# Performance work log

Measured on AMD Instinct MI355X. Metric: run time of the kernel, lower is better.

Reference implementation:

```python
import jax, jax.numpy as jnp
import numpy as np

NUM_HEADS = 16
THETA = 10000.0


def _rope(x, pos):
    # x: (B, H, S, d_k), pos: (B, S) int
    d_k = x.shape[-1]
    freqs = 1.0 / (THETA ** (jnp.arange(0, d_k, 2, dtype=jnp.float32) / d_k))  # (d_k/2,)
    angles = pos[..., None].astype(jnp.float32) * freqs  # (B, S, d_k/2)
    cos = jnp.cos(angles)[:, None, :, :]  # (B, 1, S, d_k/2) broadcast over heads
    sin = jnp.sin(angles)[:, None, :, :]
    x1 = x[..., 0::2]
    x2 = x[..., 1::2]
    out1 = x1 * cos - x2 * sin
    out2 = x1 * sin + x2 * cos
    # interleave back: (..., d_k/2, 2) -> (..., d_k)
    return jnp.stack((out1, out2), axis=-1).reshape(x.shape)


def setup_inputs() -> dict:
    key = jax.random.key(0)
    ks = jax.random.split(key, 6)
    B, S, D = 4, 2048, 1024
    x = jax.random.normal(ks[0], (B, S, D), dtype=jnp.float32)
    token_positions = jnp.sort(jax.random.randint(ks[1], (B, S), 0, S), axis=-1).astype(jnp.int32)
    Wq = jax.random.normal(ks[2], (D, D), dtype=jnp.float32) * (D ** -0.5)
    Wk = jax.random.normal(ks[3], (D, D), dtype=jnp.float32) * (D ** -0.5)
    Wv = jax.random.normal(ks[4], (D, D), dtype=jnp.float32) * (D ** -0.5)
    Wo = jax.random.normal(ks[5], (D, D), dtype=jnp.float32) * (D ** -0.5)
    return {"x": x, "token_positions": token_positions, "Wq": Wq, "Wk": Wk, "Wv": Wv, "Wo": Wo}


def reference(x, token_positions, Wq, Wk, Wv, Wo):
    B, S, D = x.shape
    H = NUM_HEADS
    d_k = D // H
    # projections: y = x @ W.T  (Linear stores weight as (d_out, d_in))
    q = jnp.einsum('bsd,od->bso', x, Wq).reshape(B, S, H, d_k).transpose(0, 2, 1, 3)
    k = jnp.einsum('bsd,od->bso', x, Wk).reshape(B, S, H, d_k).transpose(0, 2, 1, 3)
    v = jnp.einsum('bsd,od->bso', x, Wv).reshape(B, S, H, d_k).transpose(0, 2, 1, 3)
    q = _rope(q, token_positions)
    k = _rope(k, token_positions)
    scores = jnp.einsum('bhqd,bhkd->bhqk', q, k) / jnp.sqrt(jnp.float32(d_k))
    causal = jnp.tril(jnp.ones((S, S), dtype=bool))
    scores = jnp.where(causal, scores, -jnp.inf)
    attn = jax.nn.softmax(scores, axis=-1)
    attn = jnp.nan_to_num(attn, nan=0.0)
    out = jnp.einsum('bhqk,bhkd->bhqd', attn, v)
    out = out.transpose(0, 2, 1, 3).reshape(B, S, D)
    return jnp.einsum('bso,do->bsd', out, Wo)
```

## Files before the change

kernel.cpp:

```cpp
#include <hip/hip_runtime.h>
#include <stdint.h>

#define SEQ 2048
#define NH  16
#define DK  64
#define DM  1024
#define C2SM 0.18033688011112042f

typedef __bf16 bf16x8 __attribute__((ext_vector_type(8)));
typedef float  f32x4  __attribute__((ext_vector_type(4)));
typedef float  f32x16 __attribute__((ext_vector_type(16)));
typedef int    iv2    __attribute__((ext_vector_type(2)));
typedef void __attribute__((address_space(3))) lds_void;
typedef const void __attribute__((address_space(1))) glb_void;

__device__ __forceinline__ unsigned short f2b(float f) {
  unsigned int u = __float_as_uint(f);
  u += 0x7fffu + ((u >> 16) & 1u);
  return (unsigned short)(u >> 16);
}
__device__ __forceinline__ float b2f(unsigned short h) {
  return __uint_as_float(((unsigned int)h) << 16);
}
__device__ __forceinline__ void gload_lds16(const void* g, void* lds) {
  __builtin_amdgcn_global_load_lds((glb_void*)(uintptr_t)g,
                                   (lds_void*)(unsigned int)(uintptr_t)lds,
                                   16, 0, 0);
}
__device__ __forceinline__ unsigned int cvtpk(float lo, float hi) {
  unsigned int r;
  asm("v_cvt_pk_bf16_f32 %0, %1, %2" : "=v"(r) : "v"(lo), "v"(hi));
  return r;
}
__device__ __forceinline__ iv2 pl32swap(int a, int b) {
  return __builtin_amdgcn_permlane32_swap(a, b, false, false);
}

__global__ __launch_bounds__(256) void k_prep(const float* __restrict__ x,
                                              const float* __restrict__ w0,
                                              const float* __restrict__ w1,
                                              const float* __restrict__ w2,
                                              const float* __restrict__ w3,
                                              unsigned short* __restrict__ xb,
                                              unsigned short* __restrict__ wb,
                                              float2* __restrict__ tab) {
  const int bid = blockIdx.x, tid = threadIdx.x;
  if (bid < 8192) {
    int i = bid * 256 + tid;
    float4 v = ((const float4*)x)[i];
    uint2 o;
    o.x = (unsigned int)f2b(v.x) | ((unsigned int)f2b(v.y) << 16);
    o.y = (unsigned int)f2b(v.z) | ((unsigned int)f2b(v.w) << 16);
    ((uint2*)xb)[i] = o;
  } else if (bid < 12288) {
    int i = (bid - 8192) * 256 + tid;
    const float* s = (i < 524288) ? ((i < 262144) ? w0 : w1)
                                  : ((i < 786432) ? w2 : w3);
    float4 v = ((const float4*)s)[i & 262143];
    uint2 o;
    o.x = (unsigned int)f2b(v.x) | ((unsigned int)f2b(v.y) << 16);
    o.y = (unsigned int)f2b(v.z) | ((unsigned int)f2b(v.w) << 16);
    ((uint2*)wb)[i] = o;
  } else {
    int i = (bid - 12288) * 256 + tid;
    int p = i >> 5, f = i & 31;
    float freq = powf(10000.0f, -(float)(2 * f) / (float)DK);
    float ang = (float)p * freq;
    tab[i] = make_float2(cosf(ang), sinf(ang));
  }
}

template <int MODE>
__global__ __launch_bounds__(256) void k_gemm(const unsigned short* __restrict__ A,
                                              const unsigned short* __restrict__ B,
                                              void* __restrict__ C, void* __restrict__ C2,
                                              const int* __restrict__ pos,
                                              const float2* __restrict__ tab,
                                              int M, int N, int K) {
  __shared__ __align__(16) unsigned short As[3][4096];
  __shared__ __align__(16) unsigned short Bs[3][4096];
  const int tid = threadIdx.x;
  const int wid = tid >> 6, lane = tid & 63;
  const int lr = lane & 15, lk = lane >> 4;
  const int wr = wid >> 1, wc = wid & 1;
  const int m0 = blockIdx.x * 128, n0 = blockIdx.y * 128;
  const int r0 = tid >> 2;
  const int csw = (((tid & 3) ^ ((r0 >> 1) & 3)) << 3);
  const int ss = ((lk ^ ((lr >> 1) & 3)) << 3);
  f32x4 acc[4][4] = {};

#define GSTAGE(bi, k0)                                                       \
  do {                                                                       \
    gload_lds16(A + (size_t)(m0 + r0) * K + (k0) + csw, &As[bi][wid * 512]); \
    gload_lds16(A + (size_t)(m0 + 64 + r0) * K + (k0) + csw,                 \
                &As[bi][2048 + wid * 512]);                                  \
    gload_lds16(B + (size_t)(n0 + r0) * K + (k0) + csw, &Bs[bi][wid * 512]); \
    gload_lds16(B + (size_t)(n0 + 64 + r0) * K + (k0) + csw,                 \
                &Bs[bi][2048 + wid * 512]);                                  \
  } while (0)

  const int nt = K >> 5;
  GSTAGE(0, 0);
  if (nt > 1) {
    GSTAGE(1, 32);
    asm volatile("s_waitcnt vmcnt(4)" ::: "memory");
  } else {
    asm volatile("s_waitcnt vmcnt(0)" ::: "memory");
  }
  __builtin_amdgcn_s_barrier();
  int c0 = 0, c1 = 1, c2 = 2;
  for (int t = 0; t < nt; ++t) {
    if (t + 2 < nt) GSTAGE(c2, (t + 2) * 32);
    bf16x8 af[4], bfv[4];
#pragma unroll
    for (int i = 0; i < 4; ++i)
      af[i] = *(const bf16x8*)&As[c0][(wr * 64 + i * 16 + lr) * 32 + ss];
#pragma unroll
    for (int j = 0; j < 4; ++j)
      bfv[j] = *(const bf16x8*)&Bs[c0][(wc * 64 + j * 16 + lr) * 32 + ss];
    __builtin_amdgcn_s_setprio(1);
#pragma unroll
    for (int i = 0; i < 4; ++i)
#pragma unroll
      for (int j = 0; j < 4; ++j)
        acc[i][j] = __builtin_amdgcn_mfma_f32_16x16x32_bf16(af[i], bfv[j], acc[i][j], 0, 0, 0);
    __builtin_amdgcn_s_setprio(0);
    if (t + 1 < nt) {
      if (t + 2 < nt)
        asm volatile("s_waitcnt vmcnt(4)" ::: "memory");
      else
        asm volatile("s_waitcnt vmcnt(0)" ::: "memory");
      __builtin_amdgcn_s_barrier();
    }
    int tmp = c0; c0 = c1; c1 = c2; c2 = tmp;
  }
#undef GSTAGE

  if (MODE == 1) {
#pragma unroll
    for (int i = 0; i < 4; ++i) {
      const int rbase = m0 + wr * 64 + i * 16 + lk * 4;
#pragma unroll
      for (int j = 0; j < 4; ++j) {
        const int col = n0 + wc * 64 + j * 16 + lr;
#pragma unroll
        for (int r = 0; r < 4; ++r)
          ((float*)C)[(size_t)(rbase + r) * N + col] = acc[i][j][r];
      }
    }
  } else {
    const int tt = n0 >> 10;
    if (tt == 2) {
#pragma unroll
      for (int i = 0; i < 4; ++i) {
        const int rbase = m0 + wr * 64 + i * 16 + lk * 4;
        const int bb = rbase >> 11;
        const int s0 = rbase & (SEQ - 1);
#pragma unroll
        for (int j = 0; j < 4; ++j) {
          const int col = n0 + wc * 64 + j * 16 + lr;
          const int h = (col >> 6) & 15, d = col & 63;
          uint2 pv;
          pv.x = cvtpk(acc[i][j][0], acc[i][j][1]);
          pv.y = cvtpk(acc[i][j][2], acc[i][j][3]);
          *(uint2*)&((unsigned short*)C2)[(((size_t)bb * NH + h) * DK + d) * SEQ + s0] = pv;
        }
      }
    } else {
#pragma unroll
      for (int i = 0; i < 4; ++i) {
        const int rbase = m0 + wr * 64 + i * 16 + lk * 4;
        const int bb = rbase >> 11;
        int prr[4];
#pragma unroll
        for (int r = 0; r < 4; ++r)
          prr[r] = pos[bb * SEQ + ((rbase + r) & (SEQ - 1))];
#pragma unroll
        for (int j = 0; j < 4; ++j) {
          const int col = n0 + wc * 64 + j * 16 + lr;
          const int h = (col >> 6) & 15, d = col & 63;
          const int f = d >> 1;
#pragma unroll
          for (int r = 0; r < 4; ++r) {
            float v = acc[i][j][r];
            float pv = __shfl_xor(v, 1);
            float2 cs = tab[(size_t)prr[r] * 32 + f];
            float o = (d & 1) ? __builtin_fmaf(pv, cs.y, v * cs.x)
                              : __builtin_fmaf(-pv, cs.y, v * cs.x);
            const int s = (rbase + r) & (SEQ - 1);
            ((unsigned short*)C)[(size_t)tt * 8388608 +
                                 ((((size_t)bb * NH + h) * SEQ) + s) * DK + d] = f2b(o);
          }
        }
      }
    }
  }
}

__global__ __launch_bounds__(128) void k_attn(const unsigned short* __restrict__ Q,
                                              const unsigned short* __restrict__ K,
                                              const unsigned short* __restrict__ VT,
                                              unsigned short* __restrict__ O) {
  __shared__ __align__(16) unsigned short Ks[2][64 * 64];
  __shared__ __align__(16) unsigned short Vs[2][64 * 64];
  const int tid = threadIdx.x, wid = tid >> 6, lane = tid & 63;
  const int l31 = lane & 31, hi = lane >> 5;
  const int n = blockIdx.x;
  const int bh = n & 63;
  const int qt = 31 - (n >> 6);
  const unsigned short* Qp = Q + (size_t)bh * SEQ * DK;
  const unsigned short* Kp = K + (size_t)bh * SEQ * DK;
  const unsigned short* Vp = VT + (size_t)bh * DK * SEQ;
  const int b = bh >> 4, h = bh & (NH - 1);

#define STAGE(bi, kb)                                                          \
  do {                                                                         \
    _Pragma("unroll") for (int i = 0; i < 4; ++i) {                            \
      const int c = i * 128 + tid;                                             \
      const int row = c >> 3, sl = ((c & 7) ^ (row & 7)) << 3;                 \
      gload_lds16(Kp + (size_t)((kb) + row) * DK + sl,                         \
                  &Ks[bi][(i * 128 + wid * 64) * 8]);                          \
      gload_lds16(Vp + (size_t)row * SEQ + (kb) + sl,                          \
                  &Vs[bi][(i * 128 + wid * 64) * 8]);                          \
    }                                                                          \
  } while (0)

  const int qw = qt * 64 + wid * 32;
  const int qrow = qw + l31;
  bf16x8 qf[4];
#pragma unroll
  for (int ks = 0; ks < 4; ++ks)
    qf[ks] = *(const bf16x8*)&Qp[(size_t)qrow * DK + ks * 16 + hi * 8];
  f32x16 oacc[2] = {};
  float m_ = -1e30f, l_ = 0.f;
  const int ntiles = qt + 1;
  STAGE(0, 0);
  for (int kt = 0; kt < ntiles; ++kt) {
    const int cur = kt & 1;
    const int kb = kt * 64;
    if (kt + 1 < ntiles) {
      STAGE(cur ^ 1, kb + 64);
      asm volatile("s_waitcnt vmcnt(8)" ::: "memory");
    } else {
      asm volatile("s_waitcnt vmcnt(0)" ::: "memory");
    }
    __builtin_amdgcn_s_barrier();
    {
      f32x16 sa[2];
      __builtin_amdgcn_s_setprio(1);
#pragma unroll
      for (int kg = 0; kg < 2; ++kg) {
        const int krow = kg * 32 + l31;
        f32x16 z = {};
#pragma unroll
        for (int ks = 0; ks < 4; ++ks) {
          bf16x8 kf = *(const bf16x8*)((const char*)&Ks[cur][0] + krow * 128 +
                                       (((2 * ks + hi) ^ (krow & 7)) << 4));
          z = __builtin_amdgcn_mfma_f32_32x32x16_bf16(kf, qf[ks], z, 0, 0, 0);
        }
        sa[kg] = z;
      }
      __builtin_amdgcn_s_setprio(0);
      if (kb + 64 > qw) {
        const int th0 = qrow - kb - 4 * hi;
#pragma unroll
        for (int kg = 0; kg < 2; ++kg) {
          const int th = th0 - kg * 32;
#pragma unroll
          for (int r = 0; r < 16; ++r) {
            const int cst = (r & 3) + 8 * (r >> 2);
            if (cst > th) sa[kg][r] = -1e30f;
          }
        }
      }
      float mx;
      {
        float a0 = fmaxf(fmaxf(sa[0][0], sa[0][1]), fmaxf(sa[0][2], sa[0][3]));
        float a1 = fmaxf(fmaxf(sa[0][4], sa[0][5]), fmaxf(sa[0][6], sa[0][7]));
        float a2 = fmaxf(fmaxf(sa[0][8], sa[0][9]), fmaxf(sa[0][10], sa[0][11]));
        float a3 = fmaxf(fmaxf(sa[0][12], sa[0][13]), fmaxf(sa[0][14], sa[0][15]));
        float a4 = fmaxf(fmaxf(sa[1][0], sa[1][1]), fmaxf(sa[1][2], sa[1][3]));
        float a5 = fmaxf(fmaxf(sa[1][4], sa[1][5]), fmaxf(sa[1][6], sa[1][7]));
        float a6 = fmaxf(fmaxf(sa[1][8], sa[1][9]), fmaxf(sa[1][10], sa[1][11]));
        float a7 = fmaxf(fmaxf(sa[1][12], sa[1][13]), fmaxf(sa[1][14], sa[1][15]));
        mx = fmaxf(fmaxf(fmaxf(a0, a1), fmaxf(a2, a3)),
                   fmaxf(fmaxf(a4, a5), fmaxf(a6, a7)));
        iv2 t = pl32swap(__float_as_int(mx), __float_as_int(mx));
        mx = fmaxf(__int_as_float(t.x), __int_as_float(t.y));
      }
      if (!__all(mx <= m_ + 16.f)) {
        const float mn = fmaxf(m_, mx);
        const float sc = __builtin_amdgcn_exp2f((m_ - mn) * C2SM);
        m_ = mn;
        l_ *= sc;
#pragma unroll
        for (int vg = 0; vg < 2; ++vg)
#pragma unroll
          for (int r = 0; r < 16; ++r) oacc[vg][r] *= sc;
      }
      const float mc = m_ * C2SM;
      float sum = 0.f;
#pragma unroll
      for (int kg = 0; kg < 2; ++kg)
#pragma unroll
        for (int r = 0; r < 16; ++r) {
          const float p = __builtin_amdgcn_exp2f(__builtin_fmaf(sa[kg][r], C2SM, -mc));
          sa[kg][r] = p;
          sum += p;
        }
      {
        iv2 t = pl32swap(__float_as_int(sum), __float_as_int(sum));
        l_ += __int_as_float(t.x) + __int_as_float(t.y);
      }
      __builtin_amdgcn_s_setprio(1);
#pragma unroll
      for (int kg = 0; kg < 2; ++kg)
#pragma unroll
        for (int ks2 = 0; ks2 < 2; ++ks2) {
          const int rb = ks2 * 8;
          unsigned wA = cvtpk(sa[kg][rb + 0], sa[kg][rb + 1]);
          unsigned wB = cvtpk(sa[kg][rb + 4], sa[kg][rb + 5]);
          unsigned wC = cvtpk(sa[kg][rb + 2], sa[kg][rb + 3]);
          unsigned wD = cvtpk(sa[kg][rb + 6], sa[kg][rb + 7]);
          iv2 r0 = pl32swap((int)wA, (int)wB);
          iv2 r1 = pl32swap((int)wC, (int)wD);
          union { uint4 u; bf16x8 v; } pu;
          pu.u = make_uint4((unsigned)r0.x, (unsigned)r1.x, (unsigned)r0.y, (unsigned)r1.y);
          const int ks = kg * 2 + ks2;
#pragma unroll
          for (int vg = 0; vg < 2; ++vg) {
            const int vrow = vg * 32 + l31;
            bf16x8 vf = *(const bf16x8*)((const char*)&Vs[cur][0] + vrow * 128 +
                                         (((2 * ks + hi) ^ (vrow & 7)) << 4));
            oacc[vg] = __builtin_amdgcn_mfma_f32_32x32x16_bf16(vf, pu.v, oacc[vg], 0, 0, 0);
          }
        }
      __builtin_amdgcn_s_setprio(0);
    }
    __builtin_amdgcn_s_barrier();
  }
  const float inv = 1.0f / l_;
  unsigned short* Orow = O + ((size_t)(b * SEQ + qrow)) * DM + h * DK;
#pragma unroll
  for (int vg = 0; vg < 2; ++vg)
#pragma unroll
    for (int j = 0; j < 4; ++j) {
      unsigned lo = cvtpk(oacc[vg][4 * j + 0] * inv, oacc[vg][4 * j + 1] * inv);
      unsigned hh = cvtpk(oacc[vg][4 * j + 2] * inv, oacc[vg][4 * j + 3] * inv);
      *(uint2*)&Orow[vg * 32 + 8 * j + 4 * hi] = make_uint2(lo, hh);
    }
#undef STAGE
}

extern "C" void kernel_launch(void* const* d_in, const int* in_sizes, int n_in,
                              void* d_out, int out_size, void* d_ws, size_t ws_size,
                              hipStream_t stream) {
  const float* x = (const float*)d_in[0];
  const int* tp = (const int*)d_in[1];
  const float* W[4] = {(const float*)d_in[2], (const float*)d_in[3],
                       (const float*)d_in[4], (const float*)d_in[5]};
  unsigned short* xb = (unsigned short*)d_ws;
  unsigned short* wb0 = xb + (size_t)8192 * 1024;
  unsigned short* wb3 = wb0 + (size_t)3 * 1024 * 1024;
  float2* tab = (float2*)(wb0 + (size_t)4 * 1024 * 1024);
  unsigned short* Qb = (unsigned short*)(tab + SEQ * 32);
  unsigned short* Kb = Qb + (size_t)8192 * 1024;
  unsigned short* VTb = Kb + (size_t)8192 * 1024;
  unsigned short* Ob = VTb + (size_t)8192 * 1024;

  k_prep<<<12544, 256, 0, stream>>>(x, W[0], W[1], W[2], W[3], xb, wb0, tab);
  k_gemm<3><<<dim3(64, 24), 256, 0, stream>>>(xb, wb0, Qb, VTb, tp, tab, 8192, 3072, 1024);
  k_attn<<<2048, 128, 0, stream>>>(Qb, Kb, VTb, Ob);
  k_gemm<1><<<dim3(64, 8), 256, 0, stream>>>(Ob, wb3, d_out, nullptr, nullptr, nullptr,
                                             8192, 1024, 1024);
}
```

Before: 176.3 us.

## Switch GEMM to BK=64 double-buffered tiles with 8-way XOR swizzle

Moves the projection GEMM from a triple-buffered K-tile of 32 to a double-buffered K-tile of 64, with a new 8-chunk XOR swizzle on the LDS layout. Each iteration now issues twice as many async global-to-LDS loads and runs two MFMA sub-steps per barrier, halving the number of barriers and waits. The cost is shallower prefetch: only one stage is in flight, and each iteration waits for all loads to finish (vmcnt(0)) before the next, which may expose memory latency.

```diff
diff --git a/kernel.cpp b/kernel.cpp
--- a/kernel.cpp
+++ b/kernel.cpp
@@ -77,62 +77,61 @@
                                               const int* __restrict__ pos,
                                               const float2* __restrict__ tab,
                                               int M, int N, int K) {
-  __shared__ __align__(16) unsigned short As[3][4096];
-  __shared__ __align__(16) unsigned short Bs[3][4096];
+  __shared__ __align__(16) unsigned short As[2][128 * 64];
+  __shared__ __align__(16) unsigned short Bs[2][128 * 64];
   const int tid = threadIdx.x;
   const int wid = tid >> 6, lane = tid & 63;
   const int lr = lane & 15, lk = lane >> 4;
   const int wr = wid >> 1, wc = wid & 1;
   const int m0 = blockIdx.x * 128, n0 = blockIdx.y * 128;
-  const int r0 = tid >> 2;
-  const int csw = (((tid & 3) ^ ((r0 >> 1) & 3)) << 3);
-  const int ss = ((lk ^ ((lr >> 1) & 3)) << 3);
   f32x4 acc[4][4] = {};
 
-#define GSTAGE(bi, k0)                                                       \
-  do {                                                                       \
-    gload_lds16(A + (size_t)(m0 + r0) * K + (k0) + csw, &As[bi][wid * 512]); \
-    gload_lds16(A + (size_t)(m0 + 64 + r0) * K + (k0) + csw,                 \
-                &As[bi][2048 + wid * 512]);                                  \
-    gload_lds16(B + (size_t)(n0 + r0) * K + (k0) + csw, &Bs[bi][wid * 512]); \
-    gload_lds16(B + (size_t)(n0 + 64 + r0) * K + (k0) + csw,                 \
-                &Bs[bi][2048 + wid * 512]);                                  \
+#define GSTAGE(bi, k0)                                                        \
+  do {                                                                        \
+    _Pragma("unroll") for (int rp = 0; rp < 4; ++rp) {                        \
+      const int c = rp * 256 + tid;                                           \
+      const int row = c >> 3;                                                 \
+      const int sl = ((c & 7) ^ (row & 7)) << 3;                              \
+      gload_lds16(A + (size_t)(m0 + row) * K + (k0) + sl,                     \
+                  &As[bi][(rp * 256 + wid * 64) * 8]);                        \
+      gload_lds16(B + (size_t)(n0 + row) * K + (k0) + sl,                     \
+                  &Bs[bi][(rp * 256 + wid * 64) * 8]);                        \
+    }                                                                         \
   } while (0)
 
-  const int nt = K >> 5;
+  const int nt = K >> 6;
   GSTAGE(0, 0);
-  if (nt > 1) {
-    GSTAGE(1, 32);
-    asm volatile("s_waitcnt vmcnt(4)" ::: "memory");
-  } else {
+  asm volatile("s_waitcnt vmcnt(0)" ::: "memory");
+  __builtin_amdgcn_s_barrier();
+  int cur = 0;
+  for (int t = 0; t < nt; ++t) {
+    if (t + 1 < nt) GSTAGE(cur ^ 1, (t + 1) * 64);
+#pragma unroll
+    for (int kk = 0; kk < 2; ++kk) {
+      bf16x8 af[4], bfv[4];
+#pragma unroll
+      for (int i = 0; i < 4; ++i) {
+        const int rr = wr * 64 + i * 16 + lr;
+        af[i] = *(const bf16x8*)((const char*)&As[cur][0] + rr * 128 +
+                                 (((kk * 4 + lk) ^ (rr & 7)) << 4));
+      }
+#pragma unroll
+      for (int j = 0; j < 4; ++j) {
+        const int rr = wc * 64 + j * 16 + lr;
+        bfv[j] = *(const bf16x8*)((const char*)&Bs[cur][0] + rr * 128 +
+                                  (((kk * 4 + lk) ^ (rr & 7)) << 4));
+      }
+      __builtin_amdgcn_s_setprio(1);
+#pragma unroll
+      for (int i = 0; i < 4; ++i)
+#pragma unroll
+        for (int j = 0; j < 4; ++j)
+          acc[i][j] = __builtin_amdgcn_mfma_f32_16x16x32_bf16(af[i], bfv[j], acc[i][j], 0, 0, 0);
+      __builtin_amdgcn_s_setprio(0);
+    }
     asm volatile("s_waitcnt vmcnt(0)" ::: "memory");
-  }
-  __builtin_amdgcn_s_barrier();
-  int c0 = 0, c1 = 1, c2 = 2;
-  for (int t = 0; t < nt; ++t) {
-    if (t + 2 < nt) GSTAGE(c2, (t + 2) * 32);
-    bf16x8 af[4], bfv[4];
-#pragma unroll
-    for (int i = 0; i < 4; ++i)
-      af[i] = *(const bf16x8*)&As[c0][(wr * 64 + i * 16 + lr) * 32 + ss];
-#pragma unroll
-    for (int j = 0; j < 4; ++j)
-      bfv[j] = *(const bf16x8*)&Bs[c0][(wc * 64 + j * 16 + lr) * 32 + ss];
-    __builtin_amdgcn_s_setprio(1);
-#pragma unroll
-    for (int i = 0; i < 4; ++i)
-#pragma unroll
-      for (int j = 0; j < 4; ++j)
-        acc[i][j] = __builtin_amdgcn_mfma_f32_16x16x32_bf16(af[i], bfv[j], acc[i][j], 0, 0, 0);
-    __builtin_amdgcn_s_setprio(0);
-    if (t + 1 < nt) {
-      if (t + 2 < nt)
-        asm volatile("s_waitcnt vmcnt(4)" ::: "memory");
-      else
-        asm volatile("s_waitcnt vmcnt(0)" ::: "memory");
-      __builtin_amdgcn_s_barrier();
-    }
-    int tmp = c0; c0 = c1; c1 = c2; c2 = tmp;
+    __builtin_amdgcn_s_barrier();
+    cur ^= 1;
   }
 #undef GSTAGE
 
```

New measurement: 161.5 us. 8.4% less time.
